# Kernel tuning notes

Measured on AMD Instinct MI355X. Metric: run time of the kernel, lower is better.

## Reference

```python
import jax, jax.numpy as jnp
import numpy as np

INPUT_DIM = 362
HIDDEN = 256
STYLE_NUM = 60
OUTFIT_NUM = 49710
BATCH = 16384


def setup_inputs() -> dict:
    key = jax.random.key(0)
    ks = jax.random.split(key, 12)
    f32 = jnp.float32
    return {
        "i_feature": jax.random.normal(ks[0], (BATCH, INPUT_DIM), f32),
        "j_feature": jax.random.normal(ks[1], (BATCH, INPUT_DIM), f32),
        "k_feature": jax.random.normal(ks[2], (BATCH, INPUT_DIM), f32),
        # top_emb / bottom_emb Linear params (stored transposed: x @ W + b)
        "W_top": jax.random.normal(ks[3], (INPUT_DIM, HIDDEN), f32) * 0.05,
        "b_top": jnp.zeros((HIDDEN,), f32),
        "W_bot": jax.random.normal(ks[4], (INPUT_DIM, HIDDEN), f32) * 0.05,
        "b_bot": jnp.zeros((HIDDEN,), f32),
        # NMF factors (forward relu_'s them in place; we relu on use)
        "P_nmf": jax.random.normal(ks[5], (2 * INPUT_DIM, STYLE_NUM), f32),
        "N_nmf": jax.random.normal(ks[6], (2 * INPUT_DIM, STYLE_NUM), f32),
        "H1_nmf": jax.random.normal(ks[7], (STYLE_NUM, OUTFIT_NUM), f32),
        "H2_nmf": jax.random.normal(ks[8], (STYLE_NUM, OUTFIT_NUM), f32),
        "matirx_pos": jax.random.uniform(ks[9], (2 * INPUT_DIM, OUTFIT_NUM), f32),
        "matirx_neg": jax.random.uniform(ks[10], (2 * INPUT_DIM, OUTFIT_NUM), f32),
    }


def _emb(x, W, b):
    # nn.Sequential(Linear, Sigmoid)
    return jax.nn.sigmoid(x @ W + b)


def _style_score(i_f, j_f, styles, W_top, b_top, W_bot, b_bot):
    # Vectorized version of the per-sample loop:
    # squared-distance argmin codebook lookup + gather + rowwise dot.
    outfit = jnp.concatenate([i_f, j_f], axis=1)  # [B, 2D]
    # mean over feature dim of (x - s)^2; constant 1/(2D) scale does not change argmin
    d2 = (jnp.sum(outfit * outfit, axis=1, keepdims=True)
          - 2.0 * (outfit @ styles)
          + jnp.sum(styles * styles, axis=0, keepdims=True))  # [B, S]
    idx = jnp.argmin(d2, axis=1)                               # [B]
    sel = styles.T[idx]                                        # [B, 2D] gather
    top, bot = sel[:, :INPUT_DIM], sel[:, INPUT_DIM:]
    # diag(matmul) == rowwise dot
    return jnp.sum(_emb(top, W_top, b_top) * _emb(bot, W_bot, b_bot), axis=1)  # [B]


def reference(i_feature, j_feature, k_feature, W_top, b_top, W_bot, b_bot,
              P_nmf, N_nmf, H1_nmf, H2_nmf, matirx_pos, matirx_neg):
    Ti = _emb(i_feature, W_top, b_top)   # [B, H]
    Bj = _emb(j_feature, W_bot, b_bot)   # [B, H]
    Bk = _emb(k_feature, W_bot, b_bot)   # [B, H]
    # torch.diag(matmul(Ti, Bj.T)) == rowwise dot (avoids [B,B] intermediate)
    ij_score = jnp.sum(Ti * Bj, axis=1)  # [B]
    ik_score = jnp.sum(Ti * Bk, axis=1)  # [B]

    # forward does relu_ on .data before use
    P = jnp.maximum(P_nmf, 0.0)
    N = jnp.maximum(N_nmf, 0.0)
    H1 = jnp.maximum(H1_nmf, 0.0)
    H2 = jnp.maximum(H2_nmf, 0.0)

    style_ij = _style_score(i_feature, j_feature, P, W_top, b_top, W_bot, b_bot)
    style_ik = _style_score(i_feature, k_feature, N, W_top, b_top, W_bot, b_bot)

    # -mean(log(sigmoid(d))) computed stably
    loss1 = -jnp.mean(jax.nn.log_sigmoid(ij_score - ik_score))
    loss2 = -jnp.mean(jax.nn.log_sigmoid(style_ij - style_ik))
    loss3 = jnp.mean(jnp.square(matirx_pos - P @ H1)
                     + jnp.square(matirx_neg - N @ H2))
    loss = loss1 + loss2 + 0.1 * loss3

    ij_ik = jnp.stack([ij_score, ik_score], axis=1)  # [B, 2]
    auc = jnp.mean((jnp.argmax(ij_ik, axis=1) == 0).astype(jnp.float32))
    return (loss, loss1, loss2, loss3, auc)
```

## Files before the change

### kernel.cpp

```cpp
#include <hip/hip_runtime.h>
#include <math.h>

#define BATCH 16384
#define IND   362
#define KP    384
#define HID   256
#define STY   60
#define NOUT  49710
#define OUTP  49792
#define D2    724
#define D2P   768
#define NSTRIP 777
#define L3_BLOCKS (2 * NSTRIP)

typedef __bf16 bf16x8 __attribute__((ext_vector_type(8)));
typedef float  floatx4 __attribute__((ext_vector_type(4)));
typedef float  floatx2 __attribute__((ext_vector_type(2)));

__device__ inline floatx4 mfma16(bf16x8 a, bf16x8 b, floatx4 c) {
  return __builtin_amdgcn_mfma_f32_16x16x32_bf16(a, b, c, 0, 0, 0);
}

__device__ inline unsigned short f32_to_bf16(float x) {
  unsigned int u = __float_as_uint(x);
  unsigned int r = (u + 0x7FFFu + ((u >> 16) & 1u)) >> 16;
  return (unsigned short)r;
}

__device__ inline float sigm_fast(float x) { return 1.0f / (1.0f + __expf(-x)); }
__device__ inline float softplusf(float z) { return fmaxf(z, 0.0f) + log1pf(expf(-fabsf(z))); }


__global__ __launch_bounds__(256) void k_conv_feat(
    const float* __restrict__ fi, const float* __restrict__ fj,
    const float* __restrict__ fk, unsigned short* __restrict__ fbf) {
  long u = (long)blockIdx.x * 256 + threadIdx.x;
  const long TOT = (long)3 * BATCH * 48;
  if (u >= TOT) return;
  int g = (int)(u % 48);
  long rf = u / 48;
  int row = (int)(rf % BATCH);
  int f = (int)(rf / BATCH);
  const float* src = (f == 0) ? fi : (f == 1 ? fj : fk);
  int d0 = g * 8;
  const float* sp = src + (size_t)row * IND + d0;
  unsigned int wv[4];
  #pragma unroll
  for (int e = 0; e < 4; e++) {
    int dd = d0 + 2 * e;
    float lo = (dd < IND)     ? sp[2 * e]     : 0.0f;
    float hi = (dd + 1 < IND) ? sp[2 * e + 1] : 0.0f;
    wv[e] = (unsigned)f32_to_bf16(lo) | ((unsigned)f32_to_bf16(hi) << 16);
  }
  uint4 v; v.x = wv[0]; v.y = wv[1]; v.z = wv[2]; v.w = wv[3];
  *(uint4*)(fbf + ((size_t)f * BATCH + row) * KP + d0) = v;
}

__global__ void k_conv_w(const float* __restrict__ Wt, const float* __restrict__ Wb,
                         unsigned short* __restrict__ wbfT) {
  int h = blockIdx.x;
  int m = blockIdx.y;
  const float* W = m ? Wb : Wt;
  unsigned short* dst = wbfT + ((size_t)m * HID + h) * KP;
  for (int k = threadIdx.x; k < KP; k += blockDim.x) {
    float v = (k < IND) ? W[(size_t)k * HID + h] : 0.0f;
    dst[k] = f32_to_bf16(v);
  }
}

__global__ void k_conv_pn(const float* __restrict__ P, const float* __restrict__ N,
                          unsigned short* __restrict__ pnbf, unsigned short* __restrict__ pnbfT) {
  int d = blockIdx.x;
  int m = blockIdx.y;
  int s = threadIdx.x;
  const float* M = m ? N : P;
  float v = (d < D2 && s < STY) ? fmaxf(M[(size_t)d * STY + s], 0.0f) : 0.0f;
  unsigned short b = f32_to_bf16(v);
  pnbf[((size_t)m * D2P + d) * 64 + s] = b;
  int k = (d < IND) ? d : (d < D2 ? d + 22 : (d < 746 ? d - IND : d));
  pnbfT[((size_t)m * 64 + s) * D2P + k] = b;
}

__global__ void k_conv_h(const float* __restrict__ H1, const float* __restrict__ H2,
                         unsigned short* __restrict__ hbfT) {
  int o = blockIdx.x * 256 + threadIdx.x;
  int m = blockIdx.y;
  if (o >= OUTP) return;
  const float* H = m ? H2 : H1;
  unsigned short* dst = hbfT + ((size_t)m * OUTP + o) * 64;
  bool ov = (o < NOUT);
  #pragma unroll
  for (int g = 0; g < 8; g++) {
    unsigned int wv[4];
    #pragma unroll
    for (int e = 0; e < 4; e++) {
      int kk = g * 8 + e * 2;
      float lo = (ov && kk < STY)     ? fmaxf(H[(size_t)kk * NOUT + o], 0.0f) : 0.0f;
      float hi = (ov && kk + 1 < STY) ? fmaxf(H[(size_t)(kk + 1) * NOUT + o], 0.0f) : 0.0f;
      wv[e] = (unsigned)f32_to_bf16(lo) | ((unsigned)f32_to_bf16(hi) << 16);
    }
    uint4 v; v.x = wv[0]; v.y = wv[1]; v.z = wv[2]; v.w = wv[3];
    *(uint4*)(dst + g * 8) = v;
  }
}

__global__ __launch_bounds__(256) void k_style_scalar(
    const float* __restrict__ Pn, const float* __restrict__ Nn,
    const float* __restrict__ Wt, const float* __restrict__ btop,
    const float* __restrict__ Wb, const float* __restrict__ bbot,
    float* __restrict__ ss, float* __restrict__ cn) {
  int s  = blockIdx.x % STY;
  int mt = blockIdx.x / STY;
  const float* M = mt ? Nn : Pn;
  __shared__ float sel[D2];
  __shared__ float shr[4];
  int t = threadIdx.x;
  float cnp = 0.0f;
  for (int d = t; d < D2; d += 256) {
    float v = fmaxf(M[(size_t)d * STY + s], 0.0f);
    sel[d] = v;
    cnp += v * v;
  }
  __syncthreads();
  float at = btop[t], ab = bbot[t];
  for (int d = 0; d < IND; d++) at = fmaf(sel[d],        Wt[(size_t)d * HID + t], at);
  for (int d = 0; d < IND; d++) ab = fmaf(sel[IND + d],  Wb[(size_t)d * HID + t], ab);
  float prod = (1.0f / (1.0f + expf(-at))) * (1.0f / (1.0f + expf(-ab)));
  for (int off = 32; off > 0; off >>= 1) prod += __shfl_xor(prod, off);
  if ((t & 63) == 0) shr[t >> 6] = prod;
  __syncthreads();
  if (t == 0) ss[mt * 64 + s] = shr[0] + shr[1] + shr[2] + shr[3];
  __syncthreads();
  for (int off = 32; off > 0; off >>= 1) cnp += __shfl_xor(cnp, off);
  if ((t & 63) == 0) shr[t >> 6] = cnp;
  __syncthreads();
  if (t == 0) cn[mt * 64 + s] = shr[0] + shr[1] + shr[2] + shr[3];
}

__global__ __launch_bounds__(256) void k_emb(
    const unsigned short* __restrict__ fbf, const unsigned short* __restrict__ wbfT,
    const float* __restrict__ btop, const float* __restrict__ bbot,
    float* __restrict__ sIJ, float* __restrict__ sIK) {
  int w = threadIdx.x >> 6, lane = threadIdx.x & 63;
  int m = lane & 15, q = lane >> 4;
  int r0 = blockIdx.x * 64 + w * 16;
  int hb = blockIdx.y * 128;
  const unsigned short* fi = fbf + (size_t)(r0 + m) * KP + q * 8;
  const unsigned short* fj = fi + (size_t)BATCH * KP;
  const unsigned short* fk = fj + (size_t)BATCH * KP;
  floatx4 accI[8], accJ[8], accK[8];
  #pragma unroll
  for (int nt = 0; nt < 8; nt++) {
    accI[nt] = (floatx4){0.f, 0.f, 0.f, 0.f};
    accJ[nt] = (floatx4){0.f, 0.f, 0.f, 0.f};
    accK[nt] = (floatx4){0.f, 0.f, 0.f, 0.f};
  }
  for (int kc = 0; kc < 12; kc++) {
    bf16x8 ai = *(const bf16x8*)(fi + kc * 32);
    bf16x8 aj = *(const bf16x8*)(fj + kc * 32);
    bf16x8 ak = *(const bf16x8*)(fk + kc * 32);
    #pragma unroll
    for (int nt = 0; nt < 8; nt++) {
      int n = hb + nt * 16 + m;
      const unsigned short* wp = wbfT + (size_t)n * KP + kc * 32 + q * 8;
      bf16x8 bt8 = *(const bf16x8*)(wp);
      bf16x8 bb8 = *(const bf16x8*)(wp + (size_t)HID * KP);
      accI[nt] = mfma16(ai, bt8, accI[nt]);
      accJ[nt] = mfma16(aj, bb8, accJ[nt]);
      accK[nt] = mfma16(ak, bb8, accK[nt]);
    }
  }
  float sij[4] = {0.f, 0.f, 0.f, 0.f}, sik[4] = {0.f, 0.f, 0.f, 0.f};
  #pragma unroll
  for (int nt = 0; nt < 8; nt++) {
    int n = hb + nt * 16 + m;
    float vbt = btop[n], vbb = bbot[n];
    #pragma unroll
    for (int reg = 0; reg < 4; reg++) {
      float ti = sigm_fast(accI[nt][reg] + vbt);
      float tj = sigm_fast(accJ[nt][reg] + vbb);
      float tk = sigm_fast(accK[nt][reg] + vbb);
      sij[reg] += ti * tj;
      sik[reg] += ti * tk;
    }
  }
  #pragma unroll
  for (int reg = 0; reg < 4; reg++) {
    for (int off = 1; off < 16; off <<= 1) {
      sij[reg] += __shfl_xor(sij[reg], off);
      sik[reg] += __shfl_xor(sik[reg], off);
    }
  }
  if (m == 0) {
    #pragma unroll
    for (int reg = 0; reg < 4; reg++) {
      int row = r0 + q * 4 + reg;
      atomicAdd(&sIJ[row], sij[reg]);
      atomicAdd(&sIK[row], sik[reg]);
    }
  }
}

__global__ __launch_bounds__(256) void k_style_assign(
    const unsigned short* __restrict__ fbf, const unsigned short* __restrict__ pnbfT,
    const float* __restrict__ cn, const float* __restrict__ ss,
    float* __restrict__ stIJ, float* __restrict__ stIK) {
  int w = threadIdx.x >> 6, lane = threadIdx.x & 63;
  int m = lane & 15, q = lane >> 4;
  int mat = w & 1;
  int r0 = blockIdx.x * 32 + (w >> 1) * 16;
  const unsigned short* fA = fbf + (size_t)(r0 + m) * KP + q * 8;
  const unsigned short* fB = fA + (size_t)(1 + mat) * BATCH * KP;
  const unsigned short* Bp = pnbfT + (size_t)mat * 64 * D2P + q * 8;
  floatx4 acc[4];
  #pragma unroll
  for (int nt = 0; nt < 4; nt++) acc[nt] = (floatx4){0.f, 0.f, 0.f, 0.f};
  for (int kc = 0; kc < 24; kc++) {
    bf16x8 a = (kc < 12) ? *(const bf16x8*)(fA + kc * 32)
                         : *(const bf16x8*)(fB + (kc - 12) * 32);
    #pragma unroll
    for (int nt = 0; nt < 4; nt++) {
      bf16x8 b = *(const bf16x8*)(Bp + (size_t)(nt * 16 + m) * D2P + kc * 32);
      acc[nt] = mfma16(a, b, acc[nt]);
    }
  }
  const float* cnm = cn + mat * 64;
  float bv[4]; int bi[4];
  #pragma unroll
  for (int reg = 0; reg < 4; reg++) { bv[reg] = __builtin_inff(); bi[reg] = 1 << 30; }
  #pragma unroll
  for (int nt = 0; nt < 4; nt++) {
    int s = nt * 16 + m;
    float c = cnm[s & 63];
    #pragma unroll
    for (int reg = 0; reg < 4; reg++) {
      float d2 = (s < STY) ? (c - 2.0f * acc[nt][reg]) : __builtin_inff();
      if (d2 < bv[reg] || (d2 == bv[reg] && s < bi[reg])) { bv[reg] = d2; bi[reg] = s; }
    }
  }
  for (int off = 1; off < 16; off <<= 1) {
    #pragma unroll
    for (int reg = 0; reg < 4; reg++) {
      float ov = __shfl_xor(bv[reg], off);
      int   oi = __shfl_xor(bi[reg], off);
      if (ov < bv[reg] || (ov == bv[reg] && oi < bi[reg])) { bv[reg] = ov; bi[reg] = oi; }
    }
  }
  if (m == 0) {
    float* dst = mat ? stIK : stIJ;
    const float* ssm = ss + mat * 64;
    #pragma unroll
    for (int reg = 0; reg < 4; reg++) dst[r0 + q * 4 + reg] = ssm[bi[reg]];
  }
}

__global__ __launch_bounds__(256) void k_loss3(
    const unsigned short* __restrict__ pnbf, const unsigned short* __restrict__ hbfT,
    const float* __restrict__ mp, const float* __restrict__ mn,
    float* __restrict__ partial) {
  int w = threadIdx.x >> 6, lane = threadIdx.x & 63;
  int m = lane & 15, q = lane >> 4;
  int strip = blockIdx.x % NSTRIP;
  int mat   = blockIdx.x / NSTRIP;
  int o0 = strip * 64;
  const float* M = mat ? mn : mp;
  const unsigned short* Hb = hbfT + (size_t)mat * OUTP * 64;
  const unsigned short* Pb = pnbf + (size_t)mat * D2P * 64;

  bf16x8 a[4][2];
  #pragma unroll
  for (int t = 0; t < 4; t++)
    #pragma unroll
    for (int kc = 0; kc < 2; kc++)
      a[t][kc] = *(const bf16x8*)(Hb + (size_t)(o0 + t * 16 + m) * 64 + kc * 32 + q * 8);

  int dt0 = w * 12;
  int ntile = (w < 3) ? 12 : 10;
  bool full = (o0 + 64 <= NOUT);
  float local = 0.0f;

  for (int it = 0; it < ntile; it++) {
    int d0 = (dt0 + it) * 16;
    const unsigned short* bp = Pb + (size_t)(d0 + m) * 64 + q * 8;
    bf16x8 b0 = *(const bf16x8*)(bp);
    bf16x8 b1 = *(const bf16x8*)(bp + 32);
    floatx4 acc[4];
    #pragma unroll
    for (int t = 0; t < 4; t++) {
      acc[t] = (floatx4){0.f, 0.f, 0.f, 0.f};
      acc[t] = mfma16(a[t][0], b0, acc[t]);
      acc[t] = mfma16(a[t][1], b1, acc[t]);
    }
    int d = d0 + m;
    if (d < D2) {
      const float* Mrow = M + (size_t)d * NOUT;
      if (full) {
        #pragma unroll
        for (int t = 0; t < 4; t++) {
          int ob = o0 + t * 16 + q * 4;
          floatx2 m01 = *(const floatx2*)(Mrow + ob);
          floatx2 m23 = *(const floatx2*)(Mrow + ob + 2);
          float e0 = m01[0] - acc[t][0];
          float e1 = m01[1] - acc[t][1];
          float e2 = m23[0] - acc[t][2];
          float e3 = m23[1] - acc[t][3];
          local += e0 * e0 + e1 * e1 + e2 * e2 + e3 * e3;
        }
      } else {
        #pragma unroll
        for (int t = 0; t < 4; t++) {
          int ob = o0 + t * 16 + q * 4;
          #pragma unroll
          for (int reg = 0; reg < 4; reg++) {
            if (ob + reg < NOUT) {
              float e = Mrow[ob + reg] - acc[t][reg];
              local += e * e;
            }
          }
        }
      }
    }
  }
  for (int off = 32; off > 0; off >>= 1) local += __shfl_xor(local, off);
  __shared__ float shp[4];
  if (lane == 0) shp[w] = local;
  __syncthreads();
  if (threadIdx.x == 0) partial[blockIdx.x] = shp[0] + shp[1] + shp[2] + shp[3];
}

__global__ __launch_bounds__(256) void k_final(
    const float* __restrict__ sIJ, const float* __restrict__ sIK,
    const float* __restrict__ stIJ, const float* __restrict__ stIK,
    const float* __restrict__ l3partial, float* __restrict__ out) {
  int t = threadIdx.x;
  float l1 = 0.f, l2 = 0.f, ac = 0.f;
  for (int r = t; r < BATCH; r += 256) {
    float dij = sIJ[r] - sIK[r];
    l1 += softplusf(-dij);
    if (dij >= 0.0f) ac += 1.0f;
    float dst = stIJ[r] - stIK[r];
    l2 += softplusf(-dst);
  }
  double l3 = 0.0;
  for (int p = t; p < L3_BLOCKS; p += 256) l3 += (double)l3partial[p];
  __shared__ float sh1[4], sh2[4], sh3[4];
  __shared__ double sh4[4];
  for (int off = 32; off > 0; off >>= 1) {
    l1 += __shfl_xor(l1, off);
    l2 += __shfl_xor(l2, off);
    ac += __shfl_xor(ac, off);
    l3 += __shfl_xor(l3, off);
  }
  if ((t & 63) == 0) { sh1[t >> 6] = l1; sh2[t >> 6] = l2; sh3[t >> 6] = ac; sh4[t >> 6] = l3; }
  __syncthreads();
  if (t == 0) {
    double L1 = 0, L2 = 0, AC = 0, L3 = 0;
    for (int i = 0; i < 4; i++) { L1 += sh1[i]; L2 += sh2[i]; AC += sh3[i]; L3 += sh4[i]; }
    L1 /= BATCH; L2 /= BATCH; AC /= BATCH;
    L3 /= ((double)D2 * (double)NOUT);
    out[0] = (float)(L1 + L2 + 0.1 * L3);
    out[1] = (float)L1;
    out[2] = (float)L2;
    out[3] = (float)L3;
    out[4] = (float)AC;
  }
}

extern "C" void kernel_launch(void* const* d_in, const int* in_sizes, int n_in,
                              void* d_out, int out_size, void* d_ws, size_t ws_size,
                              hipStream_t stream) {
  (void)in_sizes; (void)n_in; (void)out_size; (void)ws_size;
  const float* i_f  = (const float*)d_in[0];
  const float* j_f  = (const float*)d_in[1];
  const float* k_f  = (const float*)d_in[2];
  const float* W_t  = (const float*)d_in[3];
  const float* b_t  = (const float*)d_in[4];
  const float* W_b  = (const float*)d_in[5];
  const float* b_b  = (const float*)d_in[6];
  const float* P_n  = (const float*)d_in[7];
  const float* N_n  = (const float*)d_in[8];
  const float* H1   = (const float*)d_in[9];
  const float* H2   = (const float*)d_in[10];
  const float* Mp   = (const float*)d_in[11];
  const float* Mn   = (const float*)d_in[12];
  float* out = (float*)d_out;
  char* ws = (char*)d_ws;

  const size_t OFF_FBF   = 0;
  const size_t OFF_WBFT  = OFF_FBF  + (size_t)3 * BATCH * KP * 2;
  const size_t OFF_PNBF  = OFF_WBFT + (size_t)2 * HID * KP * 2;
  const size_t OFF_PNBFT = OFF_PNBF + (size_t)2 * D2P * 64 * 2;
  const size_t OFF_HBFT  = OFF_PNBFT+ (size_t)2 * 64 * D2P * 2;
  const size_t OFF_SIJ   = OFF_HBFT + (size_t)2 * OUTP * 64 * 2;
  const size_t OFF_SIK   = OFF_SIJ  + (size_t)BATCH * 4;
  const size_t OFF_STIJ  = OFF_SIK  + (size_t)BATCH * 4;
  const size_t OFF_STIK  = OFF_STIJ + (size_t)BATCH * 4;
  const size_t OFF_SS    = OFF_STIK + (size_t)BATCH * 4;
  const size_t OFF_CN    = OFF_SS   + 512;
  const size_t OFF_L3P   = OFF_CN   + 512;

  unsigned short* fbf   = (unsigned short*)(ws + OFF_FBF);
  unsigned short* wbfT  = (unsigned short*)(ws + OFF_WBFT);
  unsigned short* pnbf  = (unsigned short*)(ws + OFF_PNBF);
  unsigned short* pnbfT = (unsigned short*)(ws + OFF_PNBFT);
  unsigned short* hbfT  = (unsigned short*)(ws + OFF_HBFT);
  float*  sIJ  = (float*)(ws + OFF_SIJ);
  float*  sIK  = (float*)(ws + OFF_SIK);
  float*  stIJ = (float*)(ws + OFF_STIJ);
  float*  stIK = (float*)(ws + OFF_STIK);
  float*  ss   = (float*)(ws + OFF_SS);
  float*  cn   = (float*)(ws + OFF_CN);
  float*  l3p  = (float*)(ws + OFF_L3P);

  hipMemsetAsync(ws + OFF_SIJ, 0, (size_t)BATCH * 4 * 2, stream);

  k_conv_feat<<<(3 * BATCH * 48 + 255) / 256, 256, 0, stream>>>(i_f, j_f, k_f, fbf);
  k_conv_w   <<<dim3(HID, 2),  128, 0, stream>>>(W_t, W_b, wbfT);
  k_conv_pn  <<<dim3(D2P, 2),   64, 0, stream>>>(P_n, N_n, pnbf, pnbfT);
  k_conv_h   <<<dim3(195, 2),  256, 0, stream>>>(H1, H2, hbfT);

  k_style_scalar<<<120, 256, 0, stream>>>(P_n, N_n, W_t, b_t, W_b, b_b, ss, cn);
  k_emb         <<<dim3(BATCH / 64, 2), 256, 0, stream>>>(fbf, wbfT, b_t, b_b, sIJ, sIK);
  k_style_assign<<<BATCH / 32, 256, 0, stream>>>(fbf, pnbfT, cn, ss, stIJ, stIK);
  k_loss3       <<<L3_BLOCKS, 256, 0, stream>>>(pnbf, hbfT, Mp, Mn, l3p);
  k_final       <<<1, 256, 0, stream>>>(sIJ, sIK, stIJ, stIK, l3p, out);
}
```

Baseline: 674.4 us.

## Merge prep kernels and main compute kernels into two launches with prefetching

Folds the five conversion and scalar style kernels into one block-partitioned prep kernel, and the loss3, embedding and style-assign kernels into one block-partitioned main kernel. This removes several launch gaps and lets the independent stages overlap on the GPU. The loss3 path also changes from contiguous per-wave tile ranges to strided tiles, and software-prefetches the next matrix row into registers. In exchange, heterogeneous blocks now share one register and occupancy budget set by the heaviest branch.

```diff
diff --git a/kernel.cpp b/kernel.cpp
--- a/kernel.cpp
+++ b/kernel.cpp
@@ -13,6 +13,17 @@
 #define NSTRIP 777
 #define L3_BLOCKS (2 * NSTRIP)
 
+#define NB_SS   120
+#define NB_CH   390
+#define NB_CW   768
+#define NB_CPN  384
+#define NB_CF   9216
+#define NB_PREP (NB_SS + NB_CH + NB_CW + NB_CPN + NB_CF)
+
+#define NB_EMB  512
+#define NB_SA   512
+#define NB_MAIN (L3_BLOCKS + NB_EMB + NB_SA)
+
 typedef __bf16 bf16x8 __attribute__((ext_vector_type(8)));
 typedef float  floatx4 __attribute__((ext_vector_type(4)));
 typedef float  floatx2 __attribute__((ext_vector_type(2)));
@@ -30,302 +41,328 @@
 __device__ inline float sigm_fast(float x) { return 1.0f / (1.0f + __expf(-x)); }
 __device__ inline float softplusf(float z) { return fmaxf(z, 0.0f) + log1pf(expf(-fabsf(z))); }
 
-
-__global__ __launch_bounds__(256) void k_conv_feat(
-    const float* __restrict__ fi, const float* __restrict__ fj,
-    const float* __restrict__ fk, unsigned short* __restrict__ fbf) {
-  long u = (long)blockIdx.x * 256 + threadIdx.x;
-  const long TOT = (long)3 * BATCH * 48;
-  if (u >= TOT) return;
-  int g = (int)(u % 48);
-  long rf = u / 48;
-  int row = (int)(rf % BATCH);
-  int f = (int)(rf / BATCH);
-  const float* src = (f == 0) ? fi : (f == 1 ? fj : fk);
-  int d0 = g * 8;
-  const float* sp = src + (size_t)row * IND + d0;
-  unsigned int wv[4];
-  #pragma unroll
-  for (int e = 0; e < 4; e++) {
-    int dd = d0 + 2 * e;
-    float lo = (dd < IND)     ? sp[2 * e]     : 0.0f;
-    float hi = (dd + 1 < IND) ? sp[2 * e + 1] : 0.0f;
-    wv[e] = (unsigned)f32_to_bf16(lo) | ((unsigned)f32_to_bf16(hi) << 16);
-  }
-  uint4 v; v.x = wv[0]; v.y = wv[1]; v.z = wv[2]; v.w = wv[3];
-  *(uint4*)(fbf + ((size_t)f * BATCH + row) * KP + d0) = v;
-}
-
-__global__ void k_conv_w(const float* __restrict__ Wt, const float* __restrict__ Wb,
-                         unsigned short* __restrict__ wbfT) {
-  int h = blockIdx.x;
-  int m = blockIdx.y;
-  const float* W = m ? Wb : Wt;
-  unsigned short* dst = wbfT + ((size_t)m * HID + h) * KP;
-  for (int k = threadIdx.x; k < KP; k += blockDim.x) {
-    float v = (k < IND) ? W[(size_t)k * HID + h] : 0.0f;
-    dst[k] = f32_to_bf16(v);
-  }
-}
-
-__global__ void k_conv_pn(const float* __restrict__ P, const float* __restrict__ N,
-                          unsigned short* __restrict__ pnbf, unsigned short* __restrict__ pnbfT) {
-  int d = blockIdx.x;
-  int m = blockIdx.y;
-  int s = threadIdx.x;
-  const float* M = m ? N : P;
-  float v = (d < D2 && s < STY) ? fmaxf(M[(size_t)d * STY + s], 0.0f) : 0.0f;
-  unsigned short b = f32_to_bf16(v);
-  pnbf[((size_t)m * D2P + d) * 64 + s] = b;
-  int k = (d < IND) ? d : (d < D2 ? d + 22 : (d < 746 ? d - IND : d));
-  pnbfT[((size_t)m * 64 + s) * D2P + k] = b;
-}
-
-__global__ void k_conv_h(const float* __restrict__ H1, const float* __restrict__ H2,
-                         unsigned short* __restrict__ hbfT) {
-  int o = blockIdx.x * 256 + threadIdx.x;
-  int m = blockIdx.y;
-  if (o >= OUTP) return;
-  const float* H = m ? H2 : H1;
-  unsigned short* dst = hbfT + ((size_t)m * OUTP + o) * 64;
-  bool ov = (o < NOUT);
-  #pragma unroll
-  for (int g = 0; g < 8; g++) {
-    unsigned int wv[4];
-    #pragma unroll
-    for (int e = 0; e < 4; e++) {
-      int kk = g * 8 + e * 2;
-      float lo = (ov && kk < STY)     ? fmaxf(H[(size_t)kk * NOUT + o], 0.0f) : 0.0f;
-      float hi = (ov && kk + 1 < STY) ? fmaxf(H[(size_t)(kk + 1) * NOUT + o], 0.0f) : 0.0f;
-      wv[e] = (unsigned)f32_to_bf16(lo) | ((unsigned)f32_to_bf16(hi) << 16);
-    }
-    uint4 v; v.x = wv[0]; v.y = wv[1]; v.z = wv[2]; v.w = wv[3];
-    *(uint4*)(dst + g * 8) = v;
-  }
-}
-
-__global__ __launch_bounds__(256) void k_style_scalar(
-    const float* __restrict__ Pn, const float* __restrict__ Nn,
+__global__ __launch_bounds__(256) void k_prep(
+    const float* __restrict__ fi, const float* __restrict__ fj, const float* __restrict__ fk,
     const float* __restrict__ Wt, const float* __restrict__ btop,
     const float* __restrict__ Wb, const float* __restrict__ bbot,
+    const float* __restrict__ Pn, const float* __restrict__ Nn,
+    const float* __restrict__ H1, const float* __restrict__ H2,
+    unsigned short* __restrict__ fbf, unsigned short* __restrict__ wbfT,
+    unsigned short* __restrict__ pnbf, unsigned short* __restrict__ pnbfT,
+    unsigned short* __restrict__ hbfT,
     float* __restrict__ ss, float* __restrict__ cn) {
-  int s  = blockIdx.x % STY;
-  int mt = blockIdx.x / STY;
-  const float* M = mt ? Nn : Pn;
   __shared__ float sel[D2];
   __shared__ float shr[4];
+  int b = blockIdx.x;
   int t = threadIdx.x;
-  float cnp = 0.0f;
-  for (int d = t; d < D2; d += 256) {
-    float v = fmaxf(M[(size_t)d * STY + s], 0.0f);
-    sel[d] = v;
-    cnp += v * v;
-  }
-  __syncthreads();
-  float at = btop[t], ab = bbot[t];
-  for (int d = 0; d < IND; d++) at = fmaf(sel[d],        Wt[(size_t)d * HID + t], at);
-  for (int d = 0; d < IND; d++) ab = fmaf(sel[IND + d],  Wb[(size_t)d * HID + t], ab);
-  float prod = (1.0f / (1.0f + expf(-at))) * (1.0f / (1.0f + expf(-ab)));
-  for (int off = 32; off > 0; off >>= 1) prod += __shfl_xor(prod, off);
-  if ((t & 63) == 0) shr[t >> 6] = prod;
-  __syncthreads();
-  if (t == 0) ss[mt * 64 + s] = shr[0] + shr[1] + shr[2] + shr[3];
-  __syncthreads();
-  for (int off = 32; off > 0; off >>= 1) cnp += __shfl_xor(cnp, off);
-  if ((t & 63) == 0) shr[t >> 6] = cnp;
-  __syncthreads();
-  if (t == 0) cn[mt * 64 + s] = shr[0] + shr[1] + shr[2] + shr[3];
-}
-
-__global__ __launch_bounds__(256) void k_emb(
+
+  if (b < NB_SS) {
+    int s  = b % STY;
+    int mt = b / STY;
+    const float* M = mt ? Nn : Pn;
+    float cnp = 0.0f;
+    for (int d = t; d < D2; d += 256) {
+      float v = fmaxf(M[(size_t)d * STY + s], 0.0f);
+      sel[d] = v;
+      cnp += v * v;
+    }
+    __syncthreads();
+    float at = btop[t], ab = bbot[t];
+    for (int d = 0; d < IND; d++) at = fmaf(sel[d],       Wt[(size_t)d * HID + t], at);
+    for (int d = 0; d < IND; d++) ab = fmaf(sel[IND + d], Wb[(size_t)d * HID + t], ab);
+    float prod = (1.0f / (1.0f + expf(-at))) * (1.0f / (1.0f + expf(-ab)));
+    for (int off = 32; off > 0; off >>= 1) prod += __shfl_xor(prod, off);
+    if ((t & 63) == 0) shr[t >> 6] = prod;
+    __syncthreads();
+    if (t == 0) ss[mt * 64 + s] = shr[0] + shr[1] + shr[2] + shr[3];
+    __syncthreads();
+    for (int off = 32; off > 0; off >>= 1) cnp += __shfl_xor(cnp, off);
+    if ((t & 63) == 0) shr[t >> 6] = cnp;
+    __syncthreads();
+    if (t == 0) cn[mt * 64 + s] = shr[0] + shr[1] + shr[2] + shr[3];
+    return;
+  }
+  b -= NB_SS;
+
+  if (b < NB_CH) {
+    int o = (b % 195) * 256 + t;
+    int m = b / 195;
+    if (o >= OUTP) return;
+    const float* H = m ? H2 : H1;
+    unsigned short* dst = hbfT + ((size_t)m * OUTP + o) * 64;
+    bool ov = (o < NOUT);
+    #pragma unroll
+    for (int g = 0; g < 8; g++) {
+      unsigned int wv[4];
+      #pragma unroll
+      for (int e = 0; e < 4; e++) {
+        int kk = g * 8 + e * 2;
+        float lo = (ov && kk < STY)     ? fmaxf(H[(size_t)kk * NOUT + o], 0.0f) : 0.0f;
+        float hi = (ov && kk + 1 < STY) ? fmaxf(H[(size_t)(kk + 1) * NOUT + o], 0.0f) : 0.0f;
+        wv[e] = (unsigned)f32_to_bf16(lo) | ((unsigned)f32_to_bf16(hi) << 16);
+      }
+      uint4 v; v.x = wv[0]; v.y = wv[1]; v.z = wv[2]; v.w = wv[3];
+      *(uint4*)(dst + g * 8) = v;
+    }
+    return;
+  }
+  b -= NB_CH;
+
+  if (b < NB_CW) {
+    int idx = b * 256 + t;
+    int k = idx % KP;
+    int rem = idx / KP;
+    int h = rem % HID;
+    int mm = rem / HID;
+    const float* W = mm ? Wb : Wt;
+    wbfT[idx] = f32_to_bf16(k < IND ? W[(size_t)k * HID + h] : 0.0f);
+    return;
+  }
+  b -= NB_CW;
+
+  if (b < NB_CPN) {
+    int u = b * 256 + t;
+    int s = u & 63;
+    int v = u >> 6;
+    int m = (v >= D2P) ? 1 : 0;
+    int d = v - m * D2P;
+    const float* M = m ? Nn : Pn;
+    float x = (d < D2 && s < STY) ? fmaxf(M[(size_t)d * STY + s], 0.0f) : 0.0f;
+    unsigned short bb = f32_to_bf16(x);
+    pnbf[((size_t)m * D2P + d) * 64 + s] = bb;
+    int k = (d < IND) ? d : (d < D2 ? d + 22 : (d < 746 ? d - IND : d));
+    pnbfT[((size_t)m * 64 + s) * D2P + k] = bb;
+    return;
+  }
+  b -= NB_CPN;
+
+  {
+    long u = (long)b * 256 + t;
+    int g = (int)(u % 48);
+    long rf = u / 48;
+    int row = (int)(rf % BATCH);
+    int f = (int)(rf / BATCH);
+    const float* src = (f == 0) ? fi : (f == 1 ? fj : fk);
+    int d0 = g * 8;
+    const float* sp = src + (size_t)row * IND + d0;
+    unsigned int wv[4];
+    #pragma unroll
+    for (int e = 0; e < 4; e++) {
+      int dd = d0 + 2 * e;
+      float lo = (dd < IND)     ? sp[2 * e]     : 0.0f;
+      float hi = (dd + 1 < IND) ? sp[2 * e + 1] : 0.0f;
+      wv[e] = (unsigned)f32_to_bf16(lo) | ((unsigned)f32_to_bf16(hi) << 16);
+    }
+    uint4 v; v.x = wv[0]; v.y = wv[1]; v.z = wv[2]; v.w = wv[3];
+    *(uint4*)(fbf + ((size_t)f * BATCH + row) * KP + d0) = v;
+  }
+}
+
+__global__ __launch_bounds__(256) void k_main(
     const unsigned short* __restrict__ fbf, const unsigned short* __restrict__ wbfT,
+    const unsigned short* __restrict__ pnbf, const unsigned short* __restrict__ pnbfT,
+    const unsigned short* __restrict__ hbfT,
     const float* __restrict__ btop, const float* __restrict__ bbot,
-    float* __restrict__ sIJ, float* __restrict__ sIK) {
+    const float* __restrict__ cn, const float* __restrict__ ss,
+    const float* __restrict__ mp, const float* __restrict__ mn,
+    float* __restrict__ sIJ, float* __restrict__ sIK,
+    float* __restrict__ stIJ, float* __restrict__ stIK,
+    float* __restrict__ partial) {
+  __shared__ float shp[4];
   int w = threadIdx.x >> 6, lane = threadIdx.x & 63;
   int m = lane & 15, q = lane >> 4;
-  int r0 = blockIdx.x * 64 + w * 16;
-  int hb = blockIdx.y * 128;
-  const unsigned short* fi = fbf + (size_t)(r0 + m) * KP + q * 8;
-  const unsigned short* fj = fi + (size_t)BATCH * KP;
-  const unsigned short* fk = fj + (size_t)BATCH * KP;
-  floatx4 accI[8], accJ[8], accK[8];
-  #pragma unroll
-  for (int nt = 0; nt < 8; nt++) {
-    accI[nt] = (floatx4){0.f, 0.f, 0.f, 0.f};
-    accJ[nt] = (floatx4){0.f, 0.f, 0.f, 0.f};
-    accK[nt] = (floatx4){0.f, 0.f, 0.f, 0.f};
-  }
-  for (int kc = 0; kc < 12; kc++) {
-    bf16x8 ai = *(const bf16x8*)(fi + kc * 32);
-    bf16x8 aj = *(const bf16x8*)(fj + kc * 32);
-    bf16x8 ak = *(const bf16x8*)(fk + kc * 32);
+  int b = blockIdx.x;
+
+  if (b < L3_BLOCKS) {
+    int strip = b % NSTRIP;
+    int mat   = b / NSTRIP;
+    int o0 = strip * 64;
+    const float* M = mat ? mn : mp;
+    const unsigned short* Hb = hbfT + (size_t)mat * OUTP * 64;
+    const unsigned short* Pb = pnbf + (size_t)mat * D2P * 64;
+
+    bf16x8 a[4][2];
+    #pragma unroll
+    for (int t = 0; t < 4; t++)
+      #pragma unroll
+      for (int kc = 0; kc < 2; kc++)
+        a[t][kc] = *(const bf16x8*)(Hb + (size_t)(o0 + t * 16 + m) * 64 + kc * 32 + q * 8);
+
+    bool full = (o0 + 64 <= NOUT);
+    float local = 0.0f;
+    floatx2 pcur[8], pnxt[8];
+    #pragma unroll
+    for (int i = 0; i < 8; i++) { pcur[i] = (floatx2){0.f, 0.f}; pnxt[i] = (floatx2){0.f, 0.f}; }
+
+    auto LOAD = [&](int dt, floatx2* dst) {
+      int d = dt * 16 + m;
+      if (d < D2) {
+        const float* Mrow = M + (size_t)d * NOUT + o0;
+        if (full) {
+          #pragma unroll
+          for (int t = 0; t < 4; t++) {
+            int ob = t * 16 + q * 4;
+            dst[2 * t]     = *(const floatx2*)(Mrow + ob);
+            dst[2 * t + 1] = *(const floatx2*)(Mrow + ob + 2);
+          }
+        } else {
+          #pragma unroll
+          for (int t = 0; t < 4; t++) {
+            int ob = t * 16 + q * 4;
+            floatx2 v0 = {0.f, 0.f}, v1 = {0.f, 0.f};
+            if (o0 + ob     < NOUT) v0[0] = Mrow[ob];
+            if (o0 + ob + 1 < NOUT) v0[1] = Mrow[ob + 1];
+            if (o0 + ob + 2 < NOUT) v1[0] = Mrow[ob + 2];
+            if (o0 + ob + 3 < NOUT) v1[1] = Mrow[ob + 3];
+            dst[2 * t] = v0; dst[2 * t + 1] = v1;
+          }
+        }
+      }
+    };
+
+    LOAD(w, pcur);
+    for (int dt = w; dt < 46; dt += 4) {
+      if (dt + 4 < 46) LOAD(dt + 4, pnxt);
+      int d0 = dt * 16;
+      const unsigned short* bp = Pb + (size_t)(d0 + m) * 64 + q * 8;
+      bf16x8 b0 = *(const bf16x8*)(bp);
+      bf16x8 b1 = *(const bf16x8*)(bp + 32);
+      floatx4 acc[4];
+      #pragma unroll
+      for (int t = 0; t < 4; t++) {
+        acc[t] = (floatx4){0.f, 0.f, 0.f, 0.f};
+        acc[t] = mfma16(a[t][0], b0, acc[t]);
+        acc[t] = mfma16(a[t][1], b1, acc[t]);
+      }
+      if (d0 + m < D2) {
+        #pragma unroll
+        for (int t = 0; t < 4; t++) {
+          float e0 = pcur[2 * t][0]     - acc[t][0];
+          float e1 = pcur[2 * t][1]     - acc[t][1];
+          float e2 = pcur[2 * t + 1][0] - acc[t][2];
+          float e3 = pcur[2 * t + 1][1] - acc[t][3];
+          local += e0 * e0 + e1 * e1 + e2 * e2 + e3 * e3;
+        }
+      }
+      #pragma unroll
+      for (int i = 0; i < 8; i++) pcur[i] = pnxt[i];
+    }
+    for (int off = 32; off > 0; off >>= 1) local += __shfl_xor(local, off);
+    if (lane == 0) shp[w] = local;
+    __syncthreads();
+    if (threadIdx.x == 0) partial[b] = shp[0] + shp[1] + shp[2] + shp[3];
+    return;
+  }
+  b -= L3_BLOCKS;
+
+  if (b < NB_EMB) {
+    int r0 = (b & 255) * 64 + w * 16;
+    int hb = (b >> 8) * 128;
+    const unsigned short* fi = fbf + (size_t)(r0 + m) * KP + q * 8;
+    const unsigned short* fj = fi + (size_t)BATCH * KP;
+    const unsigned short* fk = fj + (size_t)BATCH * KP;
+    floatx4 accI[8], accJ[8], accK[8];
+    #pragma unroll
+    for (int nt = 0; nt < 8; nt++) {
+      accI[nt] = (floatx4){0.f, 0.f, 0.f, 0.f};
+      accJ[nt] = (floatx4){0.f, 0.f, 0.f, 0.f};
+      accK[nt] = (floatx4){0.f, 0.f, 0.f, 0.f};
+    }
+    for (int kc = 0; kc < 12; kc++) {
+      bf16x8 ai = *(const bf16x8*)(fi + kc * 32);
+      bf16x8 aj = *(const bf16x8*)(fj + kc * 32);
+      bf16x8 ak = *(const bf16x8*)(fk + kc * 32);
+      #pragma unroll
+      for (int nt = 0; nt < 8; nt++) {
+        int n = hb + nt * 16 + m;
+        const unsigned short* wp = wbfT + (size_t)n * KP + kc * 32 + q * 8;
+        bf16x8 bt8 = *(const bf16x8*)(wp);
+        bf16x8 bb8 = *(const bf16x8*)(wp + (size_t)HID * KP);
+        accI[nt] = mfma16(ai, bt8, accI[nt]);
+        accJ[nt] = mfma16(aj, bb8, accJ[nt]);
+        accK[nt] = mfma16(ak, bb8, accK[nt]);
+      }
+    }
+    float sij[4] = {0.f, 0.f, 0.f, 0.f}, sik[4] = {0.f, 0.f, 0.f, 0.f};
     #pragma unroll
     for (int nt = 0; nt < 8; nt++) {
       int n = hb + nt * 16 + m;
-      const unsigned short* wp = wbfT + (size_t)n * KP + kc * 32 + q * 8;
-      bf16x8 bt8 = *(const bf16x8*)(wp);
-      bf16x8 bb8 = *(const bf16x8*)(wp + (size_t)HID * KP);
-      accI[nt] = mfma16(ai, bt8, accI[nt]);
-      accJ[nt] = mfma16(aj, bb8, accJ[nt]);
-      accK[nt] = mfma16(ak, bb8, accK[nt]);
-    }
-  }
-  float sij[4] = {0.f, 0.f, 0.f, 0.f}, sik[4] = {0.f, 0.f, 0.f, 0.f};
-  #pragma unroll
-  for (int nt = 0; nt < 8; nt++) {
-    int n = hb + nt * 16 + m;
-    float vbt = btop[n], vbb = bbot[n];
+      float vbt = btop[n], vbb = bbot[n];
+      #pragma unroll
+      for (int reg = 0; reg < 4; reg++) {
+        float ti = sigm_fast(accI[nt][reg] + vbt);
+        float tj = sigm_fast(accJ[nt][reg] + vbb);
+        float tk = sigm_fast(accK[nt][reg] + vbb);
+        sij[reg] += ti * tj;
+        sik[reg] += ti * tk;
+      }
+    }
     #pragma unroll
     for (int reg = 0; reg < 4; reg++) {
-      float ti = sigm_fast(accI[nt][reg] + vbt);
-      float tj = sigm_fast(accJ[nt][reg] + vbb);
-      float tk = sigm_fast(accK[nt][reg] + vbb);
-      sij[reg] += ti * tj;
-      sik[reg] += ti * tk;
-    }
-  }
-  #pragma unroll
-  for (int reg = 0; reg < 4; reg++) {
+      for (int off = 1; off < 16; off <<= 1) {
+        sij[reg] += __shfl_xor(sij[reg], off);
+        sik[reg] += __shfl_xor(sik[reg], off);
+      }
+    }
+    if (m == 0) {
+      #pragma unroll
+      for (int reg = 0; reg < 4; reg++) {
+        int row = r0 + q * 4 + reg;
+        atomicAdd(&sIJ[row], sij[reg]);
+        atomicAdd(&sIK[row], sik[reg]);
+      }
+    }
+    return;
+  }
+  b -= NB_EMB;
+
+  {
+    int mat = w & 1;
+    int r0 = b * 32 + (w >> 1) * 16;
+    const unsigned short* fA = fbf + (size_t)(r0 + m) * KP + q * 8;
+    const unsigned short* fB = fA + (size_t)(1 + mat) * BATCH * KP;
+    const unsigned short* Bp = pnbfT + (size_t)mat * 64 * D2P + q * 8;
+    floatx4 acc[4];
+    #pragma unroll
+    for (int nt = 0; nt < 4; nt++) acc[nt] = (floatx4){0.f, 0.f, 0.f, 0.f};
+    for (int kc = 0; kc < 24; kc++) {
+      bf16x8 a = (kc < 12) ? *(const bf16x8*)(fA + kc * 32)
+                           : *(const bf16x8*)(fB + (kc - 12) * 32);
+      #pragma unroll
+      for (int nt = 0; nt < 4; nt++) {
+        bf16x8 bb = *(const bf16x8*)(Bp + (size_t)(nt * 16 + m) * D2P + kc * 32);
+        acc[nt] = mfma16(a, bb, acc[nt]);
+      }
+    }
+    const float* cnm = cn + mat * 64;
+    float bv[4]; int bi[4];
+    #pragma unroll
+    for (int reg = 0; reg < 4; reg++) { bv[reg] = __builtin_inff(); bi[reg] = 1 << 30; }
+    #pragma unroll
+    for (int nt = 0; nt < 4; nt++) {
+      int s = nt * 16 + m;
+      float c = cnm[s & 63];
+      #pragma unroll
+      for (int reg = 0; reg < 4; reg++) {
+        float d2 = (s < STY) ? (c - 2.0f * acc[nt][reg]) : __builtin_inff();
+        if (d2 < bv[reg] || (d2 == bv[reg] && s < bi[reg])) { bv[reg] = d2; bi[reg] = s; }
+      }
+    }
     for (int off = 1; off < 16; off <<= 1) {
-      sij[reg] += __shfl_xor(sij[reg], off);
-      sik[reg] += __shfl_xor(sik[reg], off);
-    }
-  }
-  if (m == 0) {
-    #pragma unroll
-    for (int reg = 0; reg < 4; reg++) {
-      int row = r0 + q * 4 + reg;
-      atomicAdd(&sIJ[row], sij[reg]);
-      atomicAdd(&sIK[row], sik[reg]);
-    }
-  }
-}
-
-__global__ __launch_bounds__(256) void k_style_assign(
-    const unsigned short* __restrict__ fbf, const unsigned short* __restrict__ pnbfT,
-    const float* __restrict__ cn, const float* __restrict__ ss,
-    float* __restrict__ stIJ, float* __restrict__ stIK) {
-  int w = threadIdx.x >> 6, lane = threadIdx.x & 63;
-  int m = lane & 15, q = lane >> 4;
-  int mat = w & 1;
-  int r0 = blockIdx.x * 32 + (w >> 1) * 16;
-  const unsigned short* fA = fbf + (size_t)(r0 + m) * KP + q * 8;
-  const unsigned short* fB = fA + (size_t)(1 + mat) * BATCH * KP;
-  const unsigned short* Bp = pnbfT + (size_t)mat * 64 * D2P + q * 8;
-  floatx4 acc[4];
-  #pragma unroll
-  for (int nt = 0; nt < 4; nt++) acc[nt] = (floatx4){0.f, 0.f, 0.f, 0.f};
-  for (int kc = 0; kc < 24; kc++) {
-    bf16x8 a = (kc < 12) ? *(const bf16x8*)(fA + kc * 32)
-                         : *(const bf16x8*)(fB + (kc - 12) * 32);
-    #pragma unroll
-    for (int nt = 0; nt < 4; nt++) {
-      bf16x8 b = *(const bf16x8*)(Bp + (size_t)(nt * 16 + m) * D2P + kc * 32);
-      acc[nt] = mfma16(a, b, acc[nt]);
-    }
-  }
-  const float* cnm = cn + mat * 64;
-  float bv[4]; int bi[4];
-  #pragma unroll
-  for (int reg = 0; reg < 4; reg++) { bv[reg] = __builtin_inff(); bi[reg] = 1 << 30; }
-  #pragma unroll
-  for (int nt = 0; nt < 4; nt++) {
-    int s = nt * 16 + m;
-    float c = cnm[s & 63];
-    #pragma unroll
-    for (int reg = 0; reg < 4; reg++) {
-      float d2 = (s < STY) ? (c - 2.0f * acc[nt][reg]) : __builtin_inff();
-      if (d2 < bv[reg] || (d2 == bv[reg] && s < bi[reg])) { bv[reg] = d2; bi[reg] = s; }
-    }
-  }
-  for (int off = 1; off < 16; off <<= 1) {
-    #pragma unroll
-    for (int reg = 0; reg < 4; reg++) {
-      float ov = __shfl_xor(bv[reg], off);
-      int   oi = __shfl_xor(bi[reg], off);
-      if (ov < bv[reg] || (ov == bv[reg] && oi < bi[reg])) { bv[reg] = ov; bi[reg] = oi; }
-    }
-  }
-  if (m == 0) {
-    float* dst = mat ? stIK : stIJ;
-    const float* ssm = ss + mat * 64;
-    #pragma unroll
-    for (int reg = 0; reg < 4; reg++) dst[r0 + q * 4 + reg] = ssm[bi[reg]];
-  }
-}
-
-__global__ __launch_bounds__(256) void k_loss3(
-    const unsigned short* __restrict__ pnbf, const unsigned short* __restrict__ hbfT,
-    const float* __restrict__ mp, const float* __restrict__ mn,
-    float* __restrict__ partial) {
-  int w = threadIdx.x >> 6, lane = threadIdx.x & 63;
-  int m = lane & 15, q = lane >> 4;
-  int strip = blockIdx.x % NSTRIP;
-  int mat   = blockIdx.x / NSTRIP;
-  int o0 = strip * 64;
-  const float* M = mat ? mn : mp;
-  const unsigned short* Hb = hbfT + (size_t)mat * OUTP * 64;
-  const unsigned short* Pb = pnbf + (size_t)mat * D2P * 64;
-
-  bf16x8 a[4][2];
-  #pragma unroll
-  for (int t = 0; t < 4; t++)
-    #pragma unroll
-    for (int kc = 0; kc < 2; kc++)
-      a[t][kc] = *(const bf16x8*)(Hb + (size_t)(o0 + t * 16 + m) * 64 + kc * 32 + q * 8);
-
-  int dt0 = w * 12;
-  int ntile = (w < 3) ? 12 : 10;
-  bool full = (o0 + 64 <= NOUT);
-  float local = 0.0f;
-
-  for (int it = 0; it < ntile; it++) {
-    int d0 = (dt0 + it) * 16;
-    const unsigned short* bp = Pb + (size_t)(d0 + m) * 64 + q * 8;
-    bf16x8 b0 = *(const bf16x8*)(bp);
-    bf16x8 b1 = *(const bf16x8*)(bp + 32);
-    floatx4 acc[4];
-    #pragma unroll
-    for (int t = 0; t < 4; t++) {
-      acc[t] = (floatx4){0.f, 0.f, 0.f, 0.f};
-      acc[t] = mfma16(a[t][0], b0, acc[t]);
-      acc[t] = mfma16(a[t][1], b1, acc[t]);
-    }
-    int d = d0 + m;
-    if (d < D2) {
-      const float* Mrow = M + (size_t)d * NOUT;
-      if (full) {
-        #pragma unroll
-        for (int t = 0; t < 4; t++) {
-          int ob = o0 + t * 16 + q * 4;
-          floatx2 m01 = *(const floatx2*)(Mrow + ob);
-          floatx2 m23 = *(const floatx2*)(Mrow + ob + 2);
-          float e0 = m01[0] - acc[t][0];
-          float e1 = m01[1] - acc[t][1];
-          float e2 = m23[0] - acc[t][2];
-          float e3 = m23[1] - acc[t][3];
-          local += e0 * e0 + e1 * e1 + e2 * e2 + e3 * e3;
-        }
-      } else {
-        #pragma unroll
-        for (int t = 0; t < 4; t++) {
-          int ob = o0 + t * 16 + q * 4;
-          #pragma unroll
-          for (int reg = 0; reg < 4; reg++) {
-            if (ob + reg < NOUT) {
-              float e = Mrow[ob + reg] - acc[t][reg];
-              local += e * e;
-            }
-          }
-        }
-      }
-    }
-  }
-  for (int off = 32; off > 0; off >>= 1) local += __shfl_xor(local, off);
-  __shared__ float shp[4];
-  if (lane == 0) shp[w] = local;
-  __syncthreads();
-  if (threadIdx.x == 0) partial[blockIdx.x] = shp[0] + shp[1] + shp[2] + shp[3];
+      #pragma unroll
+      for (int reg = 0; reg < 4; reg++) {
+        float ov = __shfl_xor(bv[reg], off);
+        int   oi = __shfl_xor(bi[reg], off);
+        if (ov < bv[reg] || (ov == bv[reg] && oi < bi[reg])) { bv[reg] = ov; bi[reg] = oi; }
+      }
+    }
+    if (m == 0) {
+      float* dst = mat ? stIK : stIJ;
+      const float* ssm = ss + mat * 64;
+      #pragma unroll
+      for (int reg = 0; reg < 4; reg++) dst[r0 + q * 4 + reg] = ssm[bi[reg]];
+    }
+  }
 }
 
 __global__ __launch_bounds__(256) void k_final(
@@ -414,14 +451,11 @@
 
   hipMemsetAsync(ws + OFF_SIJ, 0, (size_t)BATCH * 4 * 2, stream);
 
-  k_conv_feat<<<(3 * BATCH * 48 + 255) / 256, 256, 0, stream>>>(i_f, j_f, k_f, fbf);
-  k_conv_w   <<<dim3(HID, 2),  128, 0, stream>>>(W_t, W_b, wbfT);
-  k_conv_pn  <<<dim3(D2P, 2),   64, 0, stream>>>(P_n, N_n, pnbf, pnbfT);
-  k_conv_h   <<<dim3(195, 2),  256, 0, stream>>>(H1, H2, hbfT);
-
-  k_style_scalar<<<120, 256, 0, stream>>>(P_n, N_n, W_t, b_t, W_b, b_b, ss, cn);
-  k_emb         <<<dim3(BATCH / 64, 2), 256, 0, stream>>>(fbf, wbfT, b_t, b_b, sIJ, sIK);
-  k_style_assign<<<BATCH / 32, 256, 0, stream>>>(fbf, pnbfT, cn, ss, stIJ, stIK);
-  k_loss3       <<<L3_BLOCKS, 256, 0, stream>>>(pnbf, hbfT, Mp, Mn, l3p);
-  k_final       <<<1, 256, 0, stream>>>(sIJ, sIK, stIJ, stIK, l3p, out);
-}
+  k_prep<<<NB_PREP, 256, 0, stream>>>(i_f, j_f, k_f, W_t, b_t, W_b, b_b,
+                                      P_n, N_n, H1, H2,
+                                      fbf, wbfT, pnbf, pnbfT, hbfT, ss, cn);
+  k_main<<<NB_MAIN, 256, 0, stream>>>(fbf, wbfT, pnbf, pnbfT, hbfT,
+                                      b_t, b_b, cn, ss, Mp, Mn,
+                                      sIJ, sIK, stIJ, stIK, l3p);
+  k_final<<<1, 256, 0, stream>>>(sIJ, sIK, stIJ, stIK, l3p, out);
+}
```

Result: faster. 641.9 us (-4.8%).
